# Optimization experiments

Measured on AMD Instinct MI355X. Metric: run time of the kernel, lower is better.

Reference implementation:

```python
import jax, jax.numpy as jnp
import numpy as np

# Module configuration (from init_kwargs)
N, C_IN, C_OUT, L, V, P = 4, 64, 64, 1024, 25, 3
KERNEL_SIZE, STRIDE = 9, 1
EPS = 1e-5


def _toeplitz(length):
    # Faithful to: sum_i pad(eye(L - stride*i), (i*stride, 0, 0, i*stride))
    # -> ones at [r, r + i*stride] for i in range(kernel_size // stride)
    t = jnp.zeros((length, length), dtype=jnp.float32)
    for i in range(KERNEL_SIZE // STRIDE):  # small fixed loop over taps
        t = t + jnp.eye(length, k=i * STRIDE, dtype=jnp.float32)
    return t


def setup_inputs() -> dict:
    key = jax.random.key(0)
    k0, k1, k2, k3 = jax.random.split(key, 4)
    x = jax.random.normal(k0, (N, C_IN, L, V), dtype=jnp.float32)
    A = jax.random.uniform(k1, (P, V, V), dtype=jnp.float32)
    edge_importance = jnp.ones((P, V, V), dtype=jnp.float32)
    conv_w = jax.random.normal(k2, (C_OUT * P, C_IN, 1, 1), dtype=jnp.float32) * 0.05
    conv_b = jax.random.normal(k3, (C_OUT * P,), dtype=jnp.float32) * 0.05
    gamma = jnp.ones((C_OUT,), dtype=jnp.float32)
    beta = jnp.zeros((C_OUT,), dtype=jnp.float32)
    return {"x": x, "A": A, "edge_importance": edge_importance,
            "conv_w": conv_w, "conv_b": conv_b, "gamma": gamma, "beta": beta}


def reference(x, A, edge_importance, conv_w, conv_b, gamma, beta):
    n, _, l, v = x.shape
    res = x  # residual: in_channels == out_channels and stride == 1 -> identity

    # 1x1 conv: (N, C_in, L, V) -> (N, P*C_out, L, V)
    w = conv_w[:, :, 0, 0]  # (P*C_out, C_in)
    y = jnp.einsum('nclv,kc->nklv', x, w) + conv_b[None, :, None, None]

    # split into P chunks of C_out along channels, stack, permute -> (N, L, P, C_out, V)
    y = y.reshape(n, P, C_OUT, l, v).transpose(0, 3, 1, 2, 4)

    # partition-wise graph adjacency matmul with edge-importance mask
    y = jnp.einsum('nlpcv,pvw->nlpcw', y, A * edge_importance)

    # Toeplitz temporal conv: (N, P, C, V, L) @ (L, L)
    y = y.transpose(0, 2, 3, 4, 1)
    y = jnp.matmul(y, _toeplitz(l))
    y = y.sum(axis=1)            # sum over partitions -> (N, C, V, L)
    y = y.transpose(0, 1, 3, 2)  # (N, C, L, V)

    # BatchNorm2d with batch statistics (track_running_stats=False) + ReLU
    mean = y.mean(axis=(0, 2, 3), keepdims=True)
    var = y.var(axis=(0, 2, 3), keepdims=True)  # biased, as torch uses for normalization
    y = (y - mean) * jax.lax.rsqrt(var + EPS)
    y = y * gamma[None, :, None, None] + beta[None, :, None, None]
    y = jax.nn.relu(y)

    # do = Sequential(ReLU, Dropout(0.0)) applied to (y + res)
    return jax.nn.relu(y + res)
```

## Files before the change

kernel.cpp:

```cpp
#include <hip/hip_runtime.h>


typedef unsigned short ushort_t;
typedef __attribute__((ext_vector_type(8))) short short8;
typedef __attribute__((ext_vector_type(4))) float f32x4;
typedef __attribute__((ext_vector_type(4))) unsigned short us4;
typedef __attribute__((ext_vector_type(8))) unsigned short us8;

#define N_  4
#define CI_ 64
#define CO_ 64
#define L_  1024
#define V_  25
#define P_  3
#define KS_ 9
#define NLV 102400.0f
#define NREP 128

__device__ __forceinline__ float b2f(ushort_t u) {
  union { float f; unsigned int i; } c; c.i = ((unsigned int)u) << 16; return c.f;
}
__device__ __forceinline__ ushort_t f2b(float f) {
  union { float f; unsigned int i; } c; c.f = f;
  unsigned int u = c.i;
  u += 0x7fffu + ((u >> 16) & 1u);
  return (ushort_t)(u >> 16);
}

__global__ __launch_bounds__(256) void kwin(
    const float* __restrict__ x, ushort_t* __restrict__ xs,
    const float* __restrict__ A, const float* __restrict__ E,
    const float* __restrict__ cb, const float* __restrict__ W,
    ushort_t* __restrict__ a2raw, float* __restrict__ biastab,
    ushort_t* __restrict__ wb, float* __restrict__ statsbuf)
{
  const int chunk = blockIdx.x;
  const int n = blockIdx.y;
  const int tid = threadIdx.x;

  if (chunk == 128) {
    if (n != 0) return;
    __shared__ float colA[P_ * 32];
    if (tid < P_ * 32) {
      int p = tid >> 5, w = tid & 31;
      float s = 0.f;
      if (w < V_)
        for (int v = 0; v < V_; ++v) {
          int idx = (p * V_ + v) * V_ + w;
          s += A[idx] * E[idx];
        }
      colA[tid] = s;
    }
    for (int e = tid; e < 32 * 96; e += 256) {
      int w = e / 96, k = e - w * 96;
      int p = k >> 5, v = k & 31;
      float val = 0.f;
      if (w < V_ && v < V_) {
        int idx = (p * V_ + v) * V_ + w;
        val = A[idx] * E[idx];
      }
      a2raw[e] = f2b(val);
    }
    for (int e = tid; e < 192 * 64; e += 256) wb[e] = f2b(W[e]);
    __syncthreads();
    for (int e = tid; e < 32 * 64; e += 256) {
      int w = e >> 6, c = e & 63;
      float s = 0.f;
      for (int p = 0; p < P_; ++p) s += cb[p * 64 + c] * colA[p * 32 + w];
      biastab[e] = s;
    }
    for (int e = tid; e < NREP * 128; e += 256) statsbuf[e] = 0.f;
    return;
  }

  __shared__ ushort_t tile[64 * 402];
  const int l0 = chunk * 8;
  const long xn = (long)n * CI_ * L_ * V_;
  for (int m = tid; m < 6400; m += 256) {
    int ci = m / 100;
    int j4 = (m - ci * 100) * 4;
    f32x4 d;
    if (chunk == 0 && j4 < 200) {
      d = (f32x4){0.f, 0.f, 0.f, 0.f};
    } else {
      d = *(const f32x4*)(x + xn + (long)ci * (L_ * V_) + (l0 - 8) * V_ + j4);
    }
    ushort_t* dst = &tile[ci * 402 + j4];
    dst[0] = f2b(d[0]); dst[1] = f2b(d[1]); dst[2] = f2b(d[2]); dst[3] = f2b(d[3]);
  }
  __syncthreads();
  const long xsbase = ((long)n * L_ + l0) * 1600;
  for (int cid = tid; cid < 1600; cid += 256) {
    const int v = cid >> 6, ci = cid & 63;
    const ushort_t* col = &tile[ci * 402 + v];
    float s = 0.f;
#pragma unroll
    for (int li = 0; li < 9; ++li) s += b2f(col[li * 25]);
    xs[xsbase + cid] = f2b(s);
#pragma unroll
    for (int l_ = 1; l_ < 8; ++l_) {
      s += b2f(col[(l_ + 8) * 25]) - b2f(col[(l_ - 1) * 25]);
      xs[xsbase + l_ * 1600 + cid] = f2b(s);
    }
  }
}

__global__ __launch_bounds__(256) void kmain(
    const ushort_t* __restrict__ xs,
    const ushort_t* __restrict__ Wb,
    const ushort_t* __restrict__ a2,
    const float*    __restrict__ biastab,
    ushort_t*       __restrict__ zb,
    float*          __restrict__ statsbuf)
{
  const int lb = blockIdx.x;
  const int n  = blockIdx.y;
  const int tid = threadIdx.x, lane = tid & 63, wv = tid >> 6;
  const int m16 = lane & 15, quad = lane >> 4;

  __shared__ __align__(16) ushort_t XT[4 * 2304];
  __shared__ __align__(16) ushort_t T1[2 * 13312];

  {
    const ushort_t* src = xs + ((long)n * L_ + 4 * lb) * 1600;
    for (int m = tid; m < 800; m += 256) {
      int l_ = m / 200, mr = m - l_ * 200;
      int v = mr >> 3, sub = mr & 7;
      *(us8*)(&XT[l_ * 2304 + v * 72 + sub * 8]) = *(const us8*)(src + m * 8);
    }
    if (tid < 252) {
      int l_ = tid / 63, j = tid - l_ * 63;
      *(us8*)(&XT[l_ * 2304 + 1800 + j * 8]) = (us8){0,0,0,0,0,0,0,0};
    }
  }
  __syncthreads();

  short8 af[3][2];
#pragma unroll
  for (int i = 0; i < 3; ++i) {
    const ushort_t* wrow = Wb + ((wv * 3 + i) * 16 + m16) * 64 + quad * 8;
    af[i][0] = *(const short8*)(wrow);
    af[i][1] = *(const short8*)(wrow + 32);
  }

#pragma unroll
  for (int pair = 0; pair < 2; ++pair) {
    short8 bfr[4][2];
#pragma unroll
    for (int nt = 0; nt < 4; ++nt)
#pragma unroll
      for (int ks = 0; ks < 2; ++ks)
        bfr[nt][ks] = *(const short8*)(
            &XT[(pair * 2 + (nt >> 1)) * 2304 + ((nt & 1) * 16 + m16) * 72 + ks * 32 + quad * 8]);

    f32x4 acc1[3][4];
#pragma unroll
    for (int i = 0; i < 3; ++i)
#pragma unroll
      for (int j = 0; j < 4; ++j) acc1[i][j] = (f32x4){0.f, 0.f, 0.f, 0.f};

#pragma unroll
    for (int i = 0; i < 3; ++i)
#pragma unroll
      for (int nt = 0; nt < 4; ++nt) {
        acc1[i][nt] = __builtin_amdgcn_mfma_f32_16x16x32_bf16(af[i][0], bfr[nt][0], acc1[i][nt], 0, 0, 0);
        acc1[i][nt] = __builtin_amdgcn_mfma_f32_16x16x32_bf16(af[i][1], bfr[nt][1], acc1[i][nt], 0, 0, 0);
      }
#pragma unroll
    for (int i = 0; i < 3; ++i) {
      const int mt = wv * 3 + i;
#pragma unroll
      for (int nt = 0; nt < 4; ++nt) {
        const int l_ = nt >> 1;
        const int col = (nt & 1) * 16 + m16;
#pragma unroll
        for (int r = 0; r < 4; ++r) {
          int k = mt * 16 + quad * 4 + r;
          T1[pair * 13312 + l_ * 6656 + (k & 63) * 104 + (k >> 6) * 32 + col] = f2b(acc1[i][nt][r]);
        }
      }
    }
  }
  __syncthreads();

  short8 bfr2[2][3];
#pragma unroll
  for (int nt = 0; nt < 2; ++nt)
#pragma unroll
    for (int ks = 0; ks < 3; ++ks)
      bfr2[nt][ks] = *(const short8*)(a2 + (nt * 16 + m16) * 96 + ks * 32 + quad * 8);

  const int cbase = wv * 16 + quad * 4;
  float s1[4] = {0.f, 0.f, 0.f, 0.f}, s2[4] = {0.f, 0.f, 0.f, 0.f};
#pragma unroll
  for (int pair = 0; pair < 2; ++pair) {
    f32x4 acc2[2][2];
#pragma unroll
    for (int l_ = 0; l_ < 2; ++l_)
#pragma unroll
      for (int nt = 0; nt < 2; ++nt) acc2[l_][nt] = (f32x4){0.f, 0.f, 0.f, 0.f};

#pragma unroll
    for (int l_ = 0; l_ < 2; ++l_)
#pragma unroll
      for (int ks = 0; ks < 3; ++ks) {
        short8 afT = *(const short8*)(&T1[pair * 13312 + l_ * 6656 + (wv * 16 + m16) * 104 + ks * 32 + quad * 8]);
        acc2[l_][0] = __builtin_amdgcn_mfma_f32_16x16x32_bf16(afT, bfr2[0][ks], acc2[l_][0], 0, 0, 0);
        acc2[l_][1] = __builtin_amdgcn_mfma_f32_16x16x32_bf16(afT, bfr2[1][ks], acc2[l_][1], 0, 0, 0);
      }

#pragma unroll
    for (int l_ = 0; l_ < 2; ++l_) {
      const int l = 4 * lb + pair * 2 + l_;
      const float cnt = (float)(l + 1 < KS_ ? l + 1 : KS_);
#pragma unroll
      for (int nt = 0; nt < 2; ++nt) {
        const int w = nt * 16 + m16;
        if (w < V_) {
          f32x4 bias = *(const f32x4*)(biastab + w * 64 + cbase);
          us4 pack;
#pragma unroll
          for (int r = 0; r < 4; ++r) {
            pack[r] = f2b(acc2[l_][nt][r] + cnt * bias[r]);
            float zr = b2f(pack[r]);
            s1[r] += zr; s2[r] += zr * zr;
          }
          *(us4*)(&zb[(((long)(n * L_ + l) * V_ + w) << 6) + cbase]) = pack;
        }
      }
    }
  }
#pragma unroll
  for (int off = 1; off < 16; off <<= 1) {
#pragma unroll
    for (int r = 0; r < 4; ++r) {
      s1[r] += __shfl_xor(s1[r], off, 64);
      s2[r] += __shfl_xor(s2[r], off, 64);
    }
  }
  if (m16 == 0) {
    float* sb = statsbuf + ((n * 256 + lb) & (NREP - 1)) * 128;
#pragma unroll
    for (int r = 0; r < 4; ++r) {
      atomicAdd(&sb[cbase + r], s1[r]);
      atomicAdd(&sb[64 + cbase + r], s2[r]);
    }
  }
}

__global__ __launch_bounds__(256) void kapply(
    const ushort_t* __restrict__ zb, const float* __restrict__ x,
    const float* __restrict__ statsbuf,
    const float* __restrict__ gamma, const float* __restrict__ beta,
    float* __restrict__ out)
{
  const int n = blockIdx.y, chunk = blockIdx.x;
  const int tid = threadIdx.x;
  __shared__ ushort_t zl[100 * 66];
  __shared__ float red[4][64][2];
  __shared__ float sc[64], sh[64];
  const long zbase = (long)((n * L_ + chunk * 4) * V_) * 64;
  for (int m = tid; m < 3200; m += 256) {
    int rr = m >> 5, c2 = (m & 31) * 2;
    *(unsigned int*)(&zl[rr * 66 + c2]) = ((const unsigned int*)(zb + zbase))[m];
  }
  {
    const int c = tid & 63, grp = tid >> 6;
    float a = 0.f, b = 0.f;
    for (int k = grp; k < NREP; k += 4) {
      a += statsbuf[k * 128 + c];
      b += statsbuf[k * 128 + 64 + c];
    }
    red[grp][c][0] = a;
    red[grp][c][1] = b;
  }
  __syncthreads();
  if (tid < 64) {
    const float inv = 1.0f / NLV;
    float s  = red[0][tid][0] + red[1][tid][0] + red[2][tid][0] + red[3][tid][0];
    float sq = red[0][tid][1] + red[1][tid][1] + red[2][tid][1] + red[3][tid][1];
    float mean = s * inv;
    float var  = sq * inv - mean * mean;
    float rstd = rsqrtf(var + 1e-5f);
    float g = gamma[tid];
    sc[tid] = rstd * g;
    sh[tid] = beta[tid] - mean * rstd * g;
  }
  __syncthreads();
  for (int e = tid; e < 6400; e += 256) {
    int c = e / 100, rr = e - c * 100;
    float z = b2f(zl[rr * 66 + c]);
    float y = fmaxf(z * sc[c] + sh[c], 0.f);
    long xi = ((long)(n * 64 + c) * L_ + chunk * 4) * V_ + rr;
    float o = fmaxf(y + x[xi], 0.f);
    out[xi] = o;
  }
}

extern "C" void kernel_launch(void* const* d_in, const int* in_sizes, int n_in,
                              void* d_out, int out_size, void* d_ws, size_t ws_size,
                              hipStream_t stream)
{
  const float* x     = (const float*)d_in[0];
  const float* A     = (const float*)d_in[1];
  const float* E     = (const float*)d_in[2];
  const float* W     = (const float*)d_in[3];
  const float* cb    = (const float*)d_in[4];
  const float* gamma = (const float*)d_in[5];
  const float* beta  = (const float*)d_in[6];
  float* out = (float*)d_out;

  char* ws = (char*)d_ws;
  const size_t XS_OFF   = 0;
  const size_t ZB_OFF   = 13107200;
  const size_t WB_OFF   = 26214400;
  const size_t A2_OFF   = WB_OFF + 32768;
  const size_t BIAS_OFF = A2_OFF + 16384;
  const size_t STAT_OFF = BIAS_OFF + 16384;
  ushort_t* xs      = (ushort_t*)(ws + XS_OFF);
  ushort_t* zb      = (ushort_t*)(ws + ZB_OFF);
  ushort_t* wb      = (ushort_t*)(ws + WB_OFF);
  ushort_t* a2      = (ushort_t*)(ws + A2_OFF);
  float*    biastab = (float*)(ws + BIAS_OFF);
  float*    statsbuf= (float*)(ws + STAT_OFF);

  kwin  <<<dim3(129, N_), 256, 0, stream>>>(x, xs, A, E, cb, W, a2, biastab, wb, statsbuf);
  kmain <<<dim3(256, N_), 256, 0, stream>>>(xs, wb, a2, biastab, zb, statsbuf);
  kapply<<<dim3(256, N_), 256, 0, stream>>>(zb, x, statsbuf, gamma, beta, out);
}
```

Before: 136.8 us.

## Fuse temporal window sum into main kernel and finalize BN stats in last block

The separate windowing kernel that wrote a bf16 sliding-window sum tensor to global memory is removed. Each main block now loads its own x window (12 timesteps, halo included), converts it to bf16 in LDS and computes the 9-tap running sums directly into its operand tile. The prep work is split across a small 8-block kernel. A last-block-done counter lets the final main block reduce the BN statistics into scale/shift, which the apply kernel reads directly; that kernel also uses vectorized float4 loads and stores of x and out. This removes a 13 MB round trip and per-block stats reduction, at the cost of re-reading overlapping halo rows of x and an extra grid-wide atomic.

```diff
diff --git a/kernel.cpp b/kernel.cpp
--- a/kernel.cpp
+++ b/kernel.cpp
@@ -16,6 +16,7 @@
 #define KS_ 9
 #define NLV 102400.0f
 #define NREP 128
+#define NBLK 1024
 
 __device__ __forceinline__ float b2f(ushort_t u) {
   union { float f; unsigned int i; } c; c.i = ((unsigned int)u) << 16; return c.f;
@@ -27,19 +28,15 @@
   return (ushort_t)(u >> 16);
 }
 
-__global__ __launch_bounds__(256) void kwin(
-    const float* __restrict__ x, ushort_t* __restrict__ xs,
+__global__ __launch_bounds__(256) void kprep(
     const float* __restrict__ A, const float* __restrict__ E,
-    const float* __restrict__ cb, const float* __restrict__ W,
-    ushort_t* __restrict__ a2raw, float* __restrict__ biastab,
-    ushort_t* __restrict__ wb, float* __restrict__ statsbuf)
+    const float* __restrict__ W, const float* __restrict__ cb,
+    ushort_t* __restrict__ a2, float* __restrict__ biastab,
+    ushort_t* __restrict__ wb, float* __restrict__ statsbuf,
+    unsigned int* __restrict__ counter)
 {
-  const int chunk = blockIdx.x;
-  const int n = blockIdx.y;
-  const int tid = threadIdx.x;
-
-  if (chunk == 128) {
-    if (n != 0) return;
+  const int b = blockIdx.x, tid = threadIdx.x;
+  if (b == 0) {
     __shared__ float colA[P_ * 32];
     if (tid < P_ * 32) {
       int p = tid >> 5, w = tid & 31;
@@ -51,6 +48,15 @@
         }
       colA[tid] = s;
     }
+    if (tid == 0) *counter = 0u;
+    __syncthreads();
+    for (int e = tid; e < 32 * 64; e += 256) {
+      int w = e >> 6, c = e & 63;
+      float s = 0.f;
+      for (int p = 0; p < P_; ++p) s += cb[p * 64 + c] * colA[p * 32 + w];
+      biastab[e] = s;
+    }
+  } else if (b == 1) {
     for (int e = tid; e < 32 * 96; e += 256) {
       int w = e / 96, k = e - w * 96;
       int p = k >> 5, v = k & 31;
@@ -59,59 +65,28 @@
         int idx = (p * V_ + v) * V_ + w;
         val = A[idx] * E[idx];
       }
-      a2raw[e] = f2b(val);
-    }
-    for (int e = tid; e < 192 * 64; e += 256) wb[e] = f2b(W[e]);
-    __syncthreads();
-    for (int e = tid; e < 32 * 64; e += 256) {
-      int w = e >> 6, c = e & 63;
-      float s = 0.f;
-      for (int p = 0; p < P_; ++p) s += cb[p * 64 + c] * colA[p * 32 + w];
-      biastab[e] = s;
-    }
-    for (int e = tid; e < NREP * 128; e += 256) statsbuf[e] = 0.f;
-    return;
-  }
-
-  __shared__ ushort_t tile[64 * 402];
-  const int l0 = chunk * 8;
-  const long xn = (long)n * CI_ * L_ * V_;
-  for (int m = tid; m < 6400; m += 256) {
-    int ci = m / 100;
-    int j4 = (m - ci * 100) * 4;
-    f32x4 d;
-    if (chunk == 0 && j4 < 200) {
-      d = (f32x4){0.f, 0.f, 0.f, 0.f};
-    } else {
-      d = *(const f32x4*)(x + xn + (long)ci * (L_ * V_) + (l0 - 8) * V_ + j4);
-    }
-    ushort_t* dst = &tile[ci * 402 + j4];
-    dst[0] = f2b(d[0]); dst[1] = f2b(d[1]); dst[2] = f2b(d[2]); dst[3] = f2b(d[3]);
-  }
-  __syncthreads();
-  const long xsbase = ((long)n * L_ + l0) * 1600;
-  for (int cid = tid; cid < 1600; cid += 256) {
-    const int v = cid >> 6, ci = cid & 63;
-    const ushort_t* col = &tile[ci * 402 + v];
-    float s = 0.f;
-#pragma unroll
-    for (int li = 0; li < 9; ++li) s += b2f(col[li * 25]);
-    xs[xsbase + cid] = f2b(s);
-#pragma unroll
-    for (int l_ = 1; l_ < 8; ++l_) {
-      s += b2f(col[(l_ + 8) * 25]) - b2f(col[(l_ - 1) * 25]);
-      xs[xsbase + l_ * 1600 + cid] = f2b(s);
-    }
+      a2[e] = f2b(val);
+    }
+  } else if (b < 4) {
+    const int base = (b - 2) * 6144;
+    for (int e = tid; e < 6144; e += 256) wb[base + e] = f2b(W[base + e]);
+  } else {
+    f32x4* sb = (f32x4*)statsbuf + (b - 4) * 1024;
+    for (int e = tid; e < 1024; e += 256) sb[e] = (f32x4){0.f, 0.f, 0.f, 0.f};
   }
 }
 
 __global__ __launch_bounds__(256) void kmain(
-    const ushort_t* __restrict__ xs,
+    const float*    __restrict__ x,
     const ushort_t* __restrict__ Wb,
     const ushort_t* __restrict__ a2,
     const float*    __restrict__ biastab,
     ushort_t*       __restrict__ zb,
-    float*          __restrict__ statsbuf)
+    float*          __restrict__ statsbuf,
+    unsigned int*   __restrict__ counter,
+    const float*    __restrict__ gamma,
+    const float*    __restrict__ beta,
+    float*          __restrict__ sc_sh)
 {
   const int lb = blockIdx.x;
   const int n  = blockIdx.y;
@@ -122,11 +97,36 @@
   __shared__ __align__(16) ushort_t T1[2 * 13312];
 
   {
-    const ushort_t* src = xs + ((long)n * L_ + 4 * lb) * 1600;
-    for (int m = tid; m < 800; m += 256) {
-      int l_ = m / 200, mr = m - l_ * 200;
-      int v = mr >> 3, sub = mr & 7;
-      *(us8*)(&XT[l_ * 2304 + v * 72 + sub * 8]) = *(const us8*)(src + m * 8);
+    ushort_t* tile = T1;
+    const float* xb = x + (long)n * (CI_ * L_ * V_) + (long)(4 * lb - 8) * V_;
+    const int zlim = 200 - 100 * lb;
+    for (int m = tid; m < 4800; m += 256) {
+      int ci = m / 75, j4 = (m - ci * 75) * 4;
+      f32x4 d;
+      if (j4 < zlim) d = (f32x4){0.f, 0.f, 0.f, 0.f};
+      else d = *(const f32x4*)(xb + (long)ci * (L_ * V_) + j4);
+      unsigned int p0 = ((unsigned int)f2b(d[1]) << 16) | f2b(d[0]);
+      unsigned int p1 = ((unsigned int)f2b(d[3]) << 16) | f2b(d[2]);
+      *(unsigned int*)(&tile[ci * 302 + j4])     = p0;
+      *(unsigned int*)(&tile[ci * 302 + j4 + 2]) = p1;
+    }
+  }
+  __syncthreads();
+
+  {
+    const ushort_t* tile = T1;
+    for (int cid = tid; cid < 1600; cid += 256) {
+      const int v = cid >> 6, ci = cid & 63;
+      const ushort_t* col = &tile[ci * 302 + v];
+      float s = 0.f;
+#pragma unroll
+      for (int li = 0; li < 9; ++li) s += b2f(col[li * 25]);
+      XT[v * 72 + ci] = f2b(s);
+#pragma unroll
+      for (int l_ = 1; l_ < 4; ++l_) {
+        s += b2f(col[(l_ + 8) * 25]) - b2f(col[(l_ - 1) * 25]);
+        XT[l_ * 2304 + v * 72 + ci] = f2b(s);
+      }
     }
     if (tid < 252) {
       int l_ = tid / 63, j = tid - l_ * 63;
@@ -246,54 +246,68 @@
       atomicAdd(&sb[64 + cbase + r], s2[r]);
     }
   }
+
+  __syncthreads();
+  __shared__ int lastFlag;
+  if (tid == 0) {
+    __threadfence();
+    lastFlag = (atomicAdd(counter, 1u) == (unsigned int)(NBLK - 1)) ? 1 : 0;
+  }
+  __syncthreads();
+  if (!lastFlag) return;
+
+  __threadfence();
+  __shared__ float part[256];
+  {
+    const int slot = tid & 127, half = tid >> 7;
+    float a = 0.f;
+    for (int k = half; k < NREP; k += 2)
+      a += __hip_atomic_load(&statsbuf[k * 128 + slot],
+                             __ATOMIC_RELAXED, __HIP_MEMORY_SCOPE_AGENT);
+    part[tid] = a;
+  }
+  __syncthreads();
+  if (tid < 64) {
+    const float inv = 1.0f / NLV;
+    float s    = part[tid]      + part[128 + tid];
+    float sq   = part[64 + tid] + part[192 + tid];
+    float mean = s * inv;
+    float var  = sq * inv - mean * mean;
+    float rstd = rsqrtf(var + 1e-5f);
+    float g = gamma[tid];
+    sc_sh[tid]      = rstd * g;
+    sc_sh[64 + tid] = beta[tid] - mean * rstd * g;
+  }
 }
 
 __global__ __launch_bounds__(256) void kapply(
     const ushort_t* __restrict__ zb, const float* __restrict__ x,
-    const float* __restrict__ statsbuf,
-    const float* __restrict__ gamma, const float* __restrict__ beta,
-    float* __restrict__ out)
+    const float* __restrict__ sc_sh, float* __restrict__ out)
 {
   const int n = blockIdx.y, chunk = blockIdx.x;
   const int tid = threadIdx.x;
   __shared__ ushort_t zl[100 * 66];
-  __shared__ float red[4][64][2];
   __shared__ float sc[64], sh[64];
   const long zbase = (long)((n * L_ + chunk * 4) * V_) * 64;
   for (int m = tid; m < 3200; m += 256) {
-    int rr = m >> 5, c2 = (m & 31) * 2;
-    *(unsigned int*)(&zl[rr * 66 + c2]) = ((const unsigned int*)(zb + zbase))[m];
-  }
-  {
-    const int c = tid & 63, grp = tid >> 6;
-    float a = 0.f, b = 0.f;
-    for (int k = grp; k < NREP; k += 4) {
-      a += statsbuf[k * 128 + c];
-      b += statsbuf[k * 128 + 64 + c];
-    }
-    red[grp][c][0] = a;
-    red[grp][c][1] = b;
-  }
-  __syncthreads();
-  if (tid < 64) {
-    const float inv = 1.0f / NLV;
-    float s  = red[0][tid][0] + red[1][tid][0] + red[2][tid][0] + red[3][tid][0];
-    float sq = red[0][tid][1] + red[1][tid][1] + red[2][tid][1] + red[3][tid][1];
-    float mean = s * inv;
-    float var  = sq * inv - mean * mean;
-    float rstd = rsqrtf(var + 1e-5f);
-    float g = gamma[tid];
-    sc[tid] = rstd * g;
-    sh[tid] = beta[tid] - mean * rstd * g;
-  }
-  __syncthreads();
-  for (int e = tid; e < 6400; e += 256) {
-    int c = e / 100, rr = e - c * 100;
-    float z = b2f(zl[rr * 66 + c]);
-    float y = fmaxf(z * sc[c] + sh[c], 0.f);
-    long xi = ((long)(n * 64 + c) * L_ + chunk * 4) * V_ + rr;
-    float o = fmaxf(y + x[xi], 0.f);
-    out[xi] = o;
+    *(unsigned int*)(&zl[(m >> 5) * 66 + (m & 31) * 2]) =
+        ((const unsigned int*)(zb + zbase))[m];
+  }
+  if (tid < 64) { sc[tid] = sc_sh[tid]; sh[tid] = sc_sh[64 + tid]; }
+  __syncthreads();
+  const long obase = ((long)(n * 64) * L_ + chunk * 4) * V_;
+  for (int m = tid; m < 1600; m += 256) {
+    int c = m / 25, q = m - c * 25, rr = q * 4;
+    long xi = obase + (long)c * (L_ * V_) + rr;
+    f32x4 xv = *(const f32x4*)(x + xi);
+    f32x4 o;
+#pragma unroll
+    for (int j = 0; j < 4; ++j) {
+      float z = b2f(zl[(rr + j) * 66 + c]);
+      float y = fmaxf(z * sc[c] + sh[c], 0.f);
+      o[j] = fmaxf(y + xv[j], 0.f);
+    }
+    *(f32x4*)(out + xi) = o;
   }
 }
 
@@ -311,20 +325,23 @@
   float* out = (float*)d_out;
 
   char* ws = (char*)d_ws;
-  const size_t XS_OFF   = 0;
-  const size_t ZB_OFF   = 13107200;
-  const size_t WB_OFF   = 26214400;
+  const size_t ZB_OFF   = 0;
+  const size_t WB_OFF   = 13107200;
   const size_t A2_OFF   = WB_OFF + 32768;
   const size_t BIAS_OFF = A2_OFF + 16384;
   const size_t STAT_OFF = BIAS_OFF + 16384;
-  ushort_t* xs      = (ushort_t*)(ws + XS_OFF);
-  ushort_t* zb      = (ushort_t*)(ws + ZB_OFF);
-  ushort_t* wb      = (ushort_t*)(ws + WB_OFF);
-  ushort_t* a2      = (ushort_t*)(ws + A2_OFF);
-  float*    biastab = (float*)(ws + BIAS_OFF);
-  float*    statsbuf= (float*)(ws + STAT_OFF);
-
-  kwin  <<<dim3(129, N_), 256, 0, stream>>>(x, xs, A, E, cb, W, a2, biastab, wb, statsbuf);
-  kmain <<<dim3(256, N_), 256, 0, stream>>>(xs, wb, a2, biastab, zb, statsbuf);
-  kapply<<<dim3(256, N_), 256, 0, stream>>>(zb, x, statsbuf, gamma, beta, out);
-}
+  const size_t CNT_OFF  = STAT_OFF + 65536;
+  const size_t SCSH_OFF = CNT_OFF + 256;
+  ushort_t* zb       = (ushort_t*)(ws + ZB_OFF);
+  ushort_t* wb       = (ushort_t*)(ws + WB_OFF);
+  ushort_t* a2       = (ushort_t*)(ws + A2_OFF);
+  float*    biastab  = (float*)(ws + BIAS_OFF);
+  float*    statsbuf = (float*)(ws + STAT_OFF);
+  unsigned int* counter = (unsigned int*)(ws + CNT_OFF);
+  float*    sc_sh    = (float*)(ws + SCSH_OFF);
+
+  kprep <<<dim3(8), 256, 0, stream>>>(A, E, W, cb, a2, biastab, wb, statsbuf, counter);
+  kmain <<<dim3(256, N_), 256, 0, stream>>>(x, wb, a2, biastab, zb, statsbuf,
+                                            counter, gamma, beta, sc_sh);
+  kapply<<<dim3(256, N_), 256, 0, stream>>>(zb, x, sc_sh, out);
+}
```

Result: slower. 182.6 us (+33.5%).

## Load kmain B fragments directly from global, halve T1, widen kapply chunks

Applied to the files above, without the earlier changes.

kmain no longer stages the windowed input into the XT shared-memory tile. It reads the B operands straight from global memory, zero-filling the padded vertex rows. The T1 buffer is shrunk to a single pair, with a barrier between pairs, and launch bounds request 4 blocks per CU, so LDS use drops and occupancy can rise. kapply now handles 8 time steps per block with float4 loads and stores of x and out, which should improve memory coalescing, but it relies on 16-byte alignment and doubles its shared tile.

```diff
diff --git a/kernel.cpp b/kernel.cpp
--- a/kernel.cpp
+++ b/kernel.cpp
@@ -105,7 +105,7 @@
   }
 }
 
-__global__ __launch_bounds__(256) void kmain(
+__global__ __launch_bounds__(256, 4) void kmain(
     const ushort_t* __restrict__ xs,
     const ushort_t* __restrict__ Wb,
     const ushort_t* __restrict__ a2,
@@ -118,22 +118,7 @@
   const int tid = threadIdx.x, lane = tid & 63, wv = tid >> 6;
   const int m16 = lane & 15, quad = lane >> 4;
 
-  __shared__ __align__(16) ushort_t XT[4 * 2304];
-  __shared__ __align__(16) ushort_t T1[2 * 13312];
-
-  {
-    const ushort_t* src = xs + ((long)n * L_ + 4 * lb) * 1600;
-    for (int m = tid; m < 800; m += 256) {
-      int l_ = m / 200, mr = m - l_ * 200;
-      int v = mr >> 3, sub = mr & 7;
-      *(us8*)(&XT[l_ * 2304 + v * 72 + sub * 8]) = *(const us8*)(src + m * 8);
-    }
-    if (tid < 252) {
-      int l_ = tid / 63, j = tid - l_ * 63;
-      *(us8*)(&XT[l_ * 2304 + 1800 + j * 8]) = (us8){0,0,0,0,0,0,0,0};
-    }
-  }
-  __syncthreads();
+  __shared__ __align__(16) ushort_t T1[13312];
 
   short8 af[3][2];
 #pragma unroll
@@ -143,15 +128,25 @@
     af[i][1] = *(const short8*)(wrow + 32);
   }
 
+  const ushort_t* xsb = xs + ((long)n * L_ + 4 * lb) * 1600;
+  const int cbase = wv * 16 + quad * 4;
+  float s1[4] = {0.f, 0.f, 0.f, 0.f}, s2[4] = {0.f, 0.f, 0.f, 0.f};
+
 #pragma unroll
   for (int pair = 0; pair < 2; ++pair) {
     short8 bfr[4][2];
 #pragma unroll
-    for (int nt = 0; nt < 4; ++nt)
-#pragma unroll
-      for (int ks = 0; ks < 2; ++ks)
-        bfr[nt][ks] = *(const short8*)(
-            &XT[(pair * 2 + (nt >> 1)) * 2304 + ((nt & 1) * 16 + m16) * 72 + ks * 32 + quad * 8]);
+    for (int nt = 0; nt < 4; ++nt) {
+      const int v = (nt & 1) * 16 + m16;
+      const int l_ = pair * 2 + (nt >> 1);
+#pragma unroll
+      for (int ks = 0; ks < 2; ++ks) {
+        short8 t = (short8){0, 0, 0, 0, 0, 0, 0, 0};
+        if (v < V_)
+          t = *(const short8*)(xsb + l_ * 1600 + v * 64 + ks * 32 + quad * 8);
+        bfr[nt][ks] = t;
+      }
+    }
 
     f32x4 acc1[3][4];
 #pragma unroll
@@ -166,6 +161,8 @@
         acc1[i][nt] = __builtin_amdgcn_mfma_f32_16x16x32_bf16(af[i][0], bfr[nt][0], acc1[i][nt], 0, 0, 0);
         acc1[i][nt] = __builtin_amdgcn_mfma_f32_16x16x32_bf16(af[i][1], bfr[nt][1], acc1[i][nt], 0, 0, 0);
       }
+
+    if (pair) __syncthreads();
 #pragma unroll
     for (int i = 0; i < 3; ++i) {
       const int mt = wv * 3 + i;
@@ -176,24 +173,19 @@
 #pragma unroll
         for (int r = 0; r < 4; ++r) {
           int k = mt * 16 + quad * 4 + r;
-          T1[pair * 13312 + l_ * 6656 + (k & 63) * 104 + (k >> 6) * 32 + col] = f2b(acc1[i][nt][r]);
+          T1[l_ * 6656 + (k & 63) * 104 + (k >> 6) * 32 + col] = f2b(acc1[i][nt][r]);
         }
       }
     }
-  }
-  __syncthreads();
-
-  short8 bfr2[2][3];
-#pragma unroll
-  for (int nt = 0; nt < 2; ++nt)
-#pragma unroll
-    for (int ks = 0; ks < 3; ++ks)
-      bfr2[nt][ks] = *(const short8*)(a2 + (nt * 16 + m16) * 96 + ks * 32 + quad * 8);
-
-  const int cbase = wv * 16 + quad * 4;
-  float s1[4] = {0.f, 0.f, 0.f, 0.f}, s2[4] = {0.f, 0.f, 0.f, 0.f};
-#pragma unroll
-  for (int pair = 0; pair < 2; ++pair) {
+    __syncthreads();
+
+    short8 bfr2[2][3];
+#pragma unroll
+    for (int nt = 0; nt < 2; ++nt)
+#pragma unroll
+      for (int ks = 0; ks < 3; ++ks)
+        bfr2[nt][ks] = *(const short8*)(a2 + (nt * 16 + m16) * 96 + ks * 32 + quad * 8);
+
     f32x4 acc2[2][2];
 #pragma unroll
     for (int l_ = 0; l_ < 2; ++l_)
@@ -204,7 +196,7 @@
     for (int l_ = 0; l_ < 2; ++l_)
 #pragma unroll
       for (int ks = 0; ks < 3; ++ks) {
-        short8 afT = *(const short8*)(&T1[pair * 13312 + l_ * 6656 + (wv * 16 + m16) * 104 + ks * 32 + quad * 8]);
+        short8 afT = *(const short8*)(&T1[l_ * 6656 + (wv * 16 + m16) * 104 + ks * 32 + quad * 8]);
         acc2[l_][0] = __builtin_amdgcn_mfma_f32_16x16x32_bf16(afT, bfr2[0][ks], acc2[l_][0], 0, 0, 0);
         acc2[l_][1] = __builtin_amdgcn_mfma_f32_16x16x32_bf16(afT, bfr2[1][ks], acc2[l_][1], 0, 0, 0);
       }
@@ -256,13 +248,13 @@
 {
   const int n = blockIdx.y, chunk = blockIdx.x;
   const int tid = threadIdx.x;
-  __shared__ ushort_t zl[100 * 66];
+  __shared__ ushort_t zl[200 * 66];
   __shared__ float red[4][64][2];
   __shared__ float sc[64], sh[64];
-  const long zbase = (long)((n * L_ + chunk * 4) * V_) * 64;
-  for (int m = tid; m < 3200; m += 256) {
-    int rr = m >> 5, c2 = (m & 31) * 2;
-    *(unsigned int*)(&zl[rr * 66 + c2]) = ((const unsigned int*)(zb + zbase))[m];
+  const long zbase = (long)((n * L_ + chunk * 8) * V_) * 64;
+  for (int m = tid; m < 6400; m += 256) {
+    *(unsigned int*)(&zl[(m >> 5) * 66 + (m & 31) * 2]) =
+        ((const unsigned int*)(zb + zbase))[m];
   }
   {
     const int c = tid & 63, grp = tid >> 6;
@@ -287,13 +279,19 @@
     sh[tid] = beta[tid] - mean * rstd * g;
   }
   __syncthreads();
-  for (int e = tid; e < 6400; e += 256) {
-    int c = e / 100, rr = e - c * 100;
-    float z = b2f(zl[rr * 66 + c]);
-    float y = fmaxf(z * sc[c] + sh[c], 0.f);
-    long xi = ((long)(n * 64 + c) * L_ + chunk * 4) * V_ + rr;
-    float o = fmaxf(y + x[xi], 0.f);
-    out[xi] = o;
+  const long obase = ((long)(n * 64) * L_ + chunk * 8) * V_;
+  for (int m = tid; m < 3200; m += 256) {
+    int c = m / 50, q = m - c * 50, rr = q * 4;
+    long xi = obase + (long)c * (L_ * V_) + rr;
+    f32x4 xv = *(const f32x4*)(x + xi);
+    f32x4 o;
+#pragma unroll
+    for (int j = 0; j < 4; ++j) {
+      float z = b2f(zl[(rr + j) * 66 + c]);
+      float y = fmaxf(z * sc[c] + sh[c], 0.f);
+      o[j] = fmaxf(y + xv[j], 0.f);
+    }
+    *(f32x4*)(out + xi) = o;
   }
 }
 
@@ -317,14 +315,15 @@
   const size_t A2_OFF   = WB_OFF + 32768;
   const size_t BIAS_OFF = A2_OFF + 16384;
   const size_t STAT_OFF = BIAS_OFF + 16384;
-  ushort_t* xs      = (ushort_t*)(ws + XS_OFF);
-  ushort_t* zb      = (ushort_t*)(ws + ZB_OFF);
-  ushort_t* wb      = (ushort_t*)(ws + WB_OFF);
-  ushort_t* a2      = (ushort_t*)(ws + A2_OFF);
-  float*    biastab = (float*)(ws + BIAS_OFF);
-  float*    statsbuf= (float*)(ws + STAT_OFF);
-
-  kwin  <<<dim3(129, N_), 256, 0, stream>>>(x, xs, A, E, cb, W, a2, biastab, wb, statsbuf);
+  ushort_t* xs       = (ushort_t*)(ws + XS_OFF);
+  ushort_t* zb       = (ushort_t*)(ws + ZB_OFF);
+  ushort_t* wb       = (ushort_t*)(ws + WB_OFF);
+  ushort_t* a2       = (ushort_t*)(ws + A2_OFF);
+  float*    biastab  = (float*)(ws + BIAS_OFF);
+  float*    statsbuf = (float*)(ws + STAT_OFF);
+
+  kwin  <<<dim3(129, N_), 256, 0, stream>>>(x, xs, A, E, cb, W, a2, biastab, wb,
+                                            statsbuf);
   kmain <<<dim3(256, N_), 256, 0, stream>>>(xs, wb, a2, biastab, zb, statsbuf);
-  kapply<<<dim3(256, N_), 256, 0, stream>>>(zb, x, statsbuf, gamma, beta, out);
-}
+  kapply<<<dim3(128, N_), 256, 0, stream>>>(zb, x, statsbuf, gamma, beta, out);
+}
```

Result: no change. 135.1 us (-1.2%).
